# Performance work log

Hardware: AMD Instinct MI355X
Metric: run time of the kernel (lower is better)

The kernel has to match this reference:

```python
import jax, jax.numpy as jnp
import numpy as np

N_QUBITS = 4
N_LAYERS = 2
ENT = [(i, (i + 1) % N_QUBITS) for i in range(N_QUBITS)]  # fixed entangling ring


def _ry(t):
    c, s = jnp.cos(t / 2), jnp.sin(t / 2)
    return jnp.stack([jnp.stack([c, -s]), jnp.stack([s, c])]).astype(jnp.complex64)


def _rx(t):
    c, s = jnp.cos(t / 2), jnp.sin(t / 2)
    return jnp.stack([jnp.stack([c + 0j, -1j * s]), jnp.stack([-1j * s, c + 0j])]).astype(jnp.complex64)


def _rz(t):
    e = jnp.exp(-0.5j * t.astype(jnp.complex64))
    z = jnp.zeros_like(e)
    return jnp.stack([jnp.stack([e, z]), jnp.stack([z, jnp.conj(e)])])


def _apply_1q(state, U, w):
    # state: (2,)*N_QUBITS; apply 2x2 U on wire w
    s = jnp.moveaxis(state, w, 0)
    s = jnp.tensordot(U, s, ((1,), (0,)))
    return jnp.moveaxis(s, 0, w)


def _cnot(state, c, t):
    s = jnp.moveaxis(state, (c, t), (0, 1))
    s = jnp.concatenate([s[:1], jnp.flip(s[1:], axis=1)], axis=0)
    return jnp.moveaxis(s, (0, 1), (c, t))


def _ansatz(state, vec, params):
    for i in range(N_QUBITS):
        state = _apply_1q(state, _ry(vec[i]), i)
    for l in range(N_LAYERS):
        for i in range(N_QUBITS):
            state = _apply_1q(state, _rx(params[l, i, 0]), i)
            state = _apply_1q(state, _ry(params[l, i, 1]), i)
            state = _apply_1q(state, _rz(params[l, i, 2]), i)
        for a_, b_ in ENT:
            state = _cnot(state, a_, b_)
    return state


def _adjoint_ansatz(state, vec, params):
    # inverse gates in reverse order
    for l in reversed(range(N_LAYERS)):
        for a_, b_ in reversed(ENT):
            state = _cnot(state, a_, b_)  # CNOT is self-inverse
        for i in reversed(range(N_QUBITS)):
            state = _apply_1q(state, _rz(-params[l, i, 2]), i)
            state = _apply_1q(state, _ry(-params[l, i, 1]), i)
            state = _apply_1q(state, _rx(-params[l, i, 0]), i)
    for i in reversed(range(N_QUBITS)):
        state = _apply_1q(state, _ry(-vec[i]), i)
    return state


def setup_inputs() -> dict:
    key = jax.random.key(0)
    k1, k2, k3 = jax.random.split(key, 3)
    a = jax.random.normal(k1, (1024, N_QUBITS), dtype=jnp.float32)
    b = jax.random.normal(k2, (1024, N_QUBITS), dtype=jnp.float32)
    params = jax.random.normal(k3, (N_LAYERS, N_QUBITS, 3), dtype=jnp.float32)
    return {"a": a, "b": b, "params": params}


def reference(a, b, params):
    def pair(x, y):
        psi = jnp.zeros((2,) * N_QUBITS, jnp.complex64).at[(0,) * N_QUBITS].set(1.0)
        psi = _ansatz(psi, x, params)
        psi = _adjoint_ansatz(psi, y, params)
        probs = jnp.abs(psi) ** 2
        # expval of PauliZ on wire 0: +1 for |0>, -1 for |1> on axis 0
        z = jnp.sum(probs[0]) - jnp.sum(probs[1])
        return jnp.abs(z)

    # Gram matrix [len(a), len(b)]
    return jax.vmap(lambda x: jax.vmap(lambda y: pair(x, y))(b))(a)
```

## Files before the change

kernel.cpp:

```cpp
#include <hip/hip_runtime.h>


#define NA 1024
#define NB 1024
#define KDIM 512

typedef __attribute__((ext_vector_type(8))) short bf16x8;
typedef __attribute__((ext_vector_type(4))) float f32x4;

__device__ __forceinline__ unsigned short f2bf(float x) {
    union { float f; unsigned u; } v; v.f = x;
    unsigned r = v.u + 0x7fffu + ((v.u >> 16) & 1u);
    return (unsigned short)(r >> 16);
}

__device__ __forceinline__ uint4 pack8(const float* f) {
    uint4 u;
    u.x = (unsigned)f2bf(f[0]) | ((unsigned)f2bf(f[1]) << 16);
    u.y = (unsigned)f2bf(f[2]) | ((unsigned)f2bf(f[3]) << 16);
    u.z = (unsigned)f2bf(f[4]) | ((unsigned)f2bf(f[5]) << 16);
    u.w = (unsigned)f2bf(f[6]) | ((unsigned)f2bf(f[7]) << 16);
    return u;
}

__device__ __forceinline__ void ry_gate(float* sr, float* si, int w, float t) {
    float s, c; __sincosf(0.5f * t, &s, &c);
    int st = 8 >> w;
    #pragma unroll
    for (int b = 0; b < 16; ++b) {
        if (b & st) continue;
        int j = b | st;
        float r0 = sr[b], i0 = si[b], r1 = sr[j], i1 = si[j];
        sr[b] = c * r0 - s * r1;  si[b] = c * i0 - s * i1;
        sr[j] = s * r0 + c * r1;  si[j] = s * i0 + c * i1;
    }
}

__device__ __forceinline__ void rx_gate(float* sr, float* si, int w, float t) {
    float s, c; __sincosf(0.5f * t, &s, &c);
    int st = 8 >> w;
    #pragma unroll
    for (int b = 0; b < 16; ++b) {
        if (b & st) continue;
        int j = b | st;
        float r0 = sr[b], i0 = si[b], r1 = sr[j], i1 = si[j];
        sr[b] = c * r0 + s * i1;  si[b] = c * i0 - s * r1;
        sr[j] = c * r1 + s * i0;  si[j] = c * i1 - s * r0;
    }
}

__device__ __forceinline__ void rz_gate(float* sr, float* si, int w, float t) {
    float s, c; __sincosf(0.5f * t, &s, &c);
    int st = 8 >> w;
    #pragma unroll
    for (int b = 0; b < 16; ++b) {
        if (b & st) continue;
        int j = b | st;
        float r0 = sr[b], i0 = si[b], r1 = sr[j], i1 = si[j];
        sr[b] = c * r0 + s * i0;  si[b] = c * i0 - s * r0;
        sr[j] = c * r1 - s * i1;  si[j] = c * i1 + s * r1;
    }
}

__device__ __forceinline__ void cnot_gate(float* sr, float* si, int cw, int tw) {
    int cs = 8 >> cw, ts = 8 >> tw;
    #pragma unroll
    for (int b = 0; b < 16; ++b) {
        if ((b & cs) && !(b & ts)) {
            int j = b | ts;
            float tr = sr[b]; sr[b] = sr[j]; sr[j] = tr;
            float ti = si[b]; si[b] = si[j]; si[j] = ti;
        }
    }
}

__device__ __forceinline__ void ansatz(float* sr, float* si, const float* vec, const float* P) {
    #pragma unroll
    for (int q = 0; q < 4; ++q) ry_gate(sr, si, q, vec[q]);
    #pragma unroll
    for (int l = 0; l < 2; ++l) {
        #pragma unroll
        for (int q = 0; q < 4; ++q) {
            rx_gate(sr, si, q, P[l * 12 + q * 3 + 0]);
            ry_gate(sr, si, q, P[l * 12 + q * 3 + 1]);
            rz_gate(sr, si, q, P[l * 12 + q * 3 + 2]);
        }
        cnot_gate(sr, si, 0, 1);
        cnot_gate(sr, si, 1, 2);
        cnot_gate(sr, si, 2, 3);
        cnot_gate(sr, si, 3, 0);
    }
}

__global__ __launch_bounds__(64) void qkm_phase1(
    const float* __restrict__ a, const float* __restrict__ b,
    const float* __restrict__ params,
    uint4* __restrict__ Qv, uint4* __restrict__ Mv) {
    float P[24];
    #pragma unroll
    for (int j = 0; j < 24; ++j) P[j] = params[j];
    int tid = threadIdx.x;
    int blk = blockIdx.x;

    if (blk < 256) {
        __shared__ float V[4 * 520];
        int yl = tid >> 4, p = tid & 15;
        int y = (blk << 2) + yl;
        float sr[16], si[16];
        #pragma unroll
        for (int k = 0; k < 16; ++k) { sr[k] = (k == p) ? 1.f : 0.f; si[k] = 0.f; }
        float vec[4];
        #pragma unroll
        for (int q = 0; q < 4; ++q) vec[q] = b[y * 4 + q];
        ansatz(sr, si, vec, P);
        float* row = &V[yl * 520 + p * 32];
        #pragma unroll
        for (int c = 0; c < 4; ++c) {
            *(float4*)(row + 4 * c)      = *(float4*)(sr + 4 * c);
            *(float4*)(row + 16 + 4 * c) = *(float4*)(si + 4 * c);
        }
        __syncthreads();
        int k = p;
        float mr[16], mi[16];
        #pragma unroll
        for (int l = 0; l < 16; ++l) { mr[l] = 0.f; mi[l] = 0.f; }
        #pragma unroll
        for (int p2 = 0; p2 < 16; ++p2) {
            const float* r2 = &V[yl * 520 + p2 * 32];
            float d = (p2 & 8) ? -1.f : 1.f;
            float ar = r2[k], ai = r2[16 + k];
            float dar = d * ar, dai = d * ai;
            #pragma unroll
            for (int c = 0; c < 4; ++c) {
                float4 brv = *(const float4*)(r2 + 4 * c);
                float4 biv = *(const float4*)(r2 + 16 + 4 * c);
                mr[c*4+0] += dar * brv.x + dai * biv.x;  mi[c*4+0] += dai * brv.x - dar * biv.x;
                mr[c*4+1] += dar * brv.y + dai * biv.y;  mi[c*4+1] += dai * brv.y - dar * biv.y;
                mr[c*4+2] += dar * brv.z + dai * biv.z;  mi[c*4+2] += dai * brv.z - dar * biv.z;
                mr[c*4+3] += dar * brv.w + dai * biv.w;  mi[c*4+3] += dai * brv.w - dar * biv.w;
            }
        }
        float ni[16];
        #pragma unroll
        for (int l = 0; l < 16; ++l) ni[l] = -mi[l];
        uint4* d0 = Mv + y * 64 + k * 2;
        d0[0] = pack8(&mr[0]); d0[1] = pack8(&mr[8]);
        uint4* d1 = Mv + y * 64 + 32 + k * 2;
        d1[0] = pack8(&ni[0]); d1[1] = pack8(&ni[8]);
    } else {
        int i = ((blk - 256) << 6) + tid;
        float sr[16], si[16];
        #pragma unroll
        for (int k = 0; k < 16; ++k) { sr[k] = (k == 0) ? 1.f : 0.f; si[k] = 0.f; }
        float vec[4];
        #pragma unroll
        for (int q = 0; q < 4; ++q) vec[q] = a[i * 4 + q];
        ansatz(sr, si, vec, P);
        #pragma unroll
        for (int k = 0; k < 16; ++k) {
            float t0[16], t1[16];
            float rk = sr[k], ik = si[k];
            #pragma unroll
            for (int l = 0; l < 16; ++l) {
                t0[l] = rk * sr[l] + ik * si[l];
                t1[l] = rk * si[l] - ik * sr[l];
            }
            uint4* d0 = Qv + i * 64 + k * 2;
            d0[0] = pack8(t0); d0[1] = pack8(t0 + 8);
            uint4* d1 = Qv + i * 64 + 32 + k * 2;
            d1[0] = pack8(t1); d1[1] = pack8(t1 + 8);
        }
    }
}

__global__ __launch_bounds__(256) void qkm_phase2(
    const unsigned short* __restrict__ Q, const unsigned short* __restrict__ M,
    float* __restrict__ out) {
    int wave = threadIdx.x >> 6;
    int lane = threadIdx.x & 63;
    int blk = blockIdx.x;
    int xcd = blk & 7;
    int slot = blk >> 3;
    int bi = xcd * 2 + (slot >> 4);
    int bj = slot & 15;
    int wi = wave >> 1, wj = wave & 1;
    int row0 = bi * 64 + wi * 32;
    int col0 = bj * 64 + wj * 32;
    int m16 = lane & 15;
    int quad = lane >> 4;

    const unsigned short* q0 = Q + (size_t)(row0 + m16) * KDIM + quad * 8;
    const unsigned short* q1 = q0 + 16 * KDIM;
    const unsigned short* m0 = M + (size_t)(col0 + m16) * KDIM + quad * 8;
    const unsigned short* m1 = m0 + 16 * KDIM;

    f32x4 a00 = {0.f,0.f,0.f,0.f}, a01 = {0.f,0.f,0.f,0.f};
    f32x4 a10 = {0.f,0.f,0.f,0.f}, a11 = {0.f,0.f,0.f,0.f};
    #pragma unroll 4
    for (int kk = 0; kk < 16; ++kk) {
        bf16x8 qa = *(const bf16x8*)(q0 + kk * 32);
        bf16x8 qb = *(const bf16x8*)(q1 + kk * 32);
        bf16x8 ma = *(const bf16x8*)(m0 + kk * 32);
        bf16x8 mb = *(const bf16x8*)(m1 + kk * 32);
        a00 = __builtin_amdgcn_mfma_f32_16x16x32_bf16(qa, ma, a00, 0, 0, 0);
        a01 = __builtin_amdgcn_mfma_f32_16x16x32_bf16(qa, mb, a01, 0, 0, 0);
        a10 = __builtin_amdgcn_mfma_f32_16x16x32_bf16(qb, ma, a10, 0, 0, 0);
        a11 = __builtin_amdgcn_mfma_f32_16x16x32_bf16(qb, mb, a11, 0, 0, 0);
    }
    #pragma unroll
    for (int r = 0; r < 4; ++r) {
        int r0o = row0 + quad * 4 + r;
        int r1o = r0o + 16;
        out[r0o * NB + col0 + m16]      = fabsf(a00[r]);
        out[r0o * NB + col0 + 16 + m16] = fabsf(a01[r]);
        out[r1o * NB + col0 + m16]      = fabsf(a10[r]);
        out[r1o * NB + col0 + 16 + m16] = fabsf(a11[r]);
    }
}

extern "C" void kernel_launch(void* const* d_in, const int* in_sizes, int n_in,
                              void* d_out, int out_size, void* d_ws, size_t ws_size,
                              hipStream_t stream) {
    const float* a = (const float*)d_in[0];
    const float* b = (const float*)d_in[1];
    const float* params = (const float*)d_in[2];
    float* out = (float*)d_out;

    unsigned short* Q = (unsigned short*)d_ws;
    unsigned short* M = Q + (size_t)NA * KDIM;

    qkm_phase1<<<256 + NA / 64, 64, 0, stream>>>(a, b, params, (uint4*)Q, (uint4*)M);
    qkm_phase2<<<256, 256, 0, stream>>>(Q, M, out);
}
```

Baseline: 75.65 us.

## Halve GEMM K by exploiting Hermitian symmetry of density and observable matrices

```diff
diff --git a/kernel.cpp b/kernel.cpp
--- a/kernel.cpp
+++ b/kernel.cpp
@@ -3,7 +3,8 @@
 
 #define NA 1024
 #define NB 1024
-#define KDIM 512
+#define KD 256
+#define RT2 1.41421356237f
 
 typedef __attribute__((ext_vector_type(8))) short bf16x8;
 typedef __attribute__((ext_vector_type(4))) float f32x4;
@@ -102,53 +103,49 @@
     int tid = threadIdx.x;
     int blk = blockIdx.x;
 
-    if (blk < 256) {
-        __shared__ float V[4 * 520];
-        int yl = tid >> 4, p = tid & 15;
-        int y = (blk << 2) + yl;
+    if (blk < 128) {
+        __shared__ float Wr[16][64];
+        __shared__ float Wi[16][64];
+        int g = tid >> 3, t = tid & 7;
+        int y = (blk << 3) + g;
         float sr[16], si[16];
         #pragma unroll
-        for (int k = 0; k < 16; ++k) { sr[k] = (k == p) ? 1.f : 0.f; si[k] = 0.f; }
+        for (int k = 0; k < 16; ++k) { sr[k] = (k == 8 + t) ? 1.f : 0.f; si[k] = 0.f; }
         float vec[4];
         #pragma unroll
         for (int q = 0; q < 4; ++q) vec[q] = b[y * 4 + q];
         ansatz(sr, si, vec, P);
-        float* row = &V[yl * 520 + p * 32];
-        #pragma unroll
-        for (int c = 0; c < 4; ++c) {
-            *(float4*)(row + 4 * c)      = *(float4*)(sr + 4 * c);
-            *(float4*)(row + 16 + 4 * c) = *(float4*)(si + 4 * c);
-        }
+        #pragma unroll
+        for (int l = 0; l < 16; ++l) { Wr[l][tid] = sr[l]; Wi[l][tid] = si[l]; }
         __syncthreads();
-        int k = p;
-        float mr[16], mi[16];
-        #pragma unroll
-        for (int l = 0; l < 16; ++l) { mr[l] = 0.f; mi[l] = 0.f; }
-        #pragma unroll
-        for (int p2 = 0; p2 < 16; ++p2) {
-            const float* r2 = &V[yl * 520 + p2 * 32];
-            float d = (p2 & 8) ? -1.f : 1.f;
-            float ar = r2[k], ai = r2[16 + k];
-            float dar = d * ar, dai = d * ai;
-            #pragma unroll
-            for (int c = 0; c < 4; ++c) {
-                float4 brv = *(const float4*)(r2 + 4 * c);
-                float4 biv = *(const float4*)(r2 + 16 + 4 * c);
-                mr[c*4+0] += dar * brv.x + dai * biv.x;  mi[c*4+0] += dai * brv.x - dar * biv.x;
-                mr[c*4+1] += dar * brv.y + dai * biv.y;  mi[c*4+1] += dai * brv.y - dar * biv.y;
-                mr[c*4+2] += dar * brv.z + dai * biv.z;  mi[c*4+2] += dai * brv.z - dar * biv.z;
-                mr[c*4+3] += dar * brv.w + dai * biv.w;  mi[c*4+3] += dai * brv.w - dar * biv.w;
+        int base = g << 3;
+        #pragma unroll
+        for (int kr = 0; kr < 2; ++kr) {
+            int k = 2 * t + kr;
+            float re[16], im[16];
+            #pragma unroll
+            for (int l = 0; l < 16; ++l) { re[l] = 0.f; im[l] = 0.f; }
+            #pragma unroll
+            for (int p2 = 0; p2 < 8; ++p2) {
+                float wrk = Wr[k][base + p2], wik = Wi[k][base + p2];
+                #pragma unroll
+                for (int l = 0; l < 16; ++l) {
+                    float wrl = Wr[l][base + p2], wil = Wi[l][base + p2];
+                    re[l] += wrk * wrl + wik * wil;
+                    im[l] += wil * wrk - wrl * wik;
+                }
             }
-        }
-        float ni[16];
-        #pragma unroll
-        for (int l = 0; l < 16; ++l) ni[l] = -mi[l];
-        uint4* d0 = Mv + y * 64 + k * 2;
-        d0[0] = pack8(&mr[0]); d0[1] = pack8(&mr[8]);
-        uint4* d1 = Mv + y * 64 + 32 + k * 2;
-        d1[0] = pack8(&ni[0]); d1[1] = pack8(&ni[8]);
-    } else {
-        int i = ((blk - 256) << 6) + tid;
+            float row[16];
+            #pragma unroll
+            for (int l = 0; l < 16; ++l) {
+                float off = (l < k) ? im[l] : re[l];
+                row[l] = (l == k) ? (1.f - 2.f * re[l]) : (-2.f * RT2 * off);
+            }
+            uint4* d = Mv + y * 32 + k * 2;
+            d[0] = pack8(row); d[1] = pack8(row + 8);
+        }
+    } else if (blk < 144) {
+        int i = ((blk - 128) << 6) + tid;
         float sr[16], si[16];
         #pragma unroll
         for (int k = 0; k < 16; ++k) { sr[k] = (k == 0) ? 1.f : 0.f; si[k] = 0.f; }
@@ -158,17 +155,16 @@
         ansatz(sr, si, vec, P);
         #pragma unroll
         for (int k = 0; k < 16; ++k) {
-            float t0[16], t1[16];
             float rk = sr[k], ik = si[k];
+            float row[16];
             #pragma unroll
             for (int l = 0; l < 16; ++l) {
-                t0[l] = rk * sr[l] + ik * si[l];
-                t1[l] = rk * si[l] - ik * sr[l];
+                if (l < k)       row[l] = RT2 * (si[l] * rk - sr[l] * ik);
+                else if (l == k) row[l] = rk * rk + ik * ik;
+                else             row[l] = RT2 * (rk * sr[l] + ik * si[l]);
             }
-            uint4* d0 = Qv + i * 64 + k * 2;
-            d0[0] = pack8(t0); d0[1] = pack8(t0 + 8);
-            uint4* d1 = Qv + i * 64 + 32 + k * 2;
-            d1[0] = pack8(t1); d1[1] = pack8(t1 + 8);
+            uint4* d = Qv + i * 32 + k * 2;
+            d[0] = pack8(row); d[1] = pack8(row + 8);
         }
     }
 }
@@ -189,15 +185,15 @@
     int m16 = lane & 15;
     int quad = lane >> 4;
 
-    const unsigned short* q0 = Q + (size_t)(row0 + m16) * KDIM + quad * 8;
-    const unsigned short* q1 = q0 + 16 * KDIM;
-    const unsigned short* m0 = M + (size_t)(col0 + m16) * KDIM + quad * 8;
-    const unsigned short* m1 = m0 + 16 * KDIM;
+    const unsigned short* q0 = Q + (size_t)(row0 + m16) * KD + quad * 8;
+    const unsigned short* q1 = q0 + 16 * KD;
+    const unsigned short* m0 = M + (size_t)(col0 + m16) * KD + quad * 8;
+    const unsigned short* m1 = m0 + 16 * KD;
 
     f32x4 a00 = {0.f,0.f,0.f,0.f}, a01 = {0.f,0.f,0.f,0.f};
     f32x4 a10 = {0.f,0.f,0.f,0.f}, a11 = {0.f,0.f,0.f,0.f};
-    #pragma unroll 4
-    for (int kk = 0; kk < 16; ++kk) {
+    #pragma unroll
+    for (int kk = 0; kk < 8; ++kk) {
         bf16x8 qa = *(const bf16x8*)(q0 + kk * 32);
         bf16x8 qb = *(const bf16x8*)(q1 + kk * 32);
         bf16x8 ma = *(const bf16x8*)(m0 + kk * 32);
@@ -227,8 +223,8 @@
     float* out = (float*)d_out;
 
     unsigned short* Q = (unsigned short*)d_ws;
-    unsigned short* M = Q + (size_t)NA * KDIM;
-
-    qkm_phase1<<<256 + NA / 64, 64, 0, stream>>>(a, b, params, (uint4*)Q, (uint4*)M);
+    unsigned short* M = Q + (size_t)NA * KD;
+
+    qkm_phase1<<<144, 64, 0, stream>>>(a, b, params, (uint4*)Q, (uint4*)M);
     qkm_phase2<<<256, 256, 0, stream>>>(Q, M, out);
 }
```

New measurement: 70.83 us. 6.4% less time.
